# Performance work log

Hardware: AMD Instinct MI355X
Metric: run time of the kernel (lower is better)

The kernel has to match this reference:

```python
import jax, jax.numpy as jnp
import numpy as np

N = 4096            # data_length
T_IN, D_IN = 64, 128
F = 32 * 64         # target_length * output_dim


def setup_inputs() -> dict:
    key = jax.random.key(0)
    k1, k2, k3, k4 = jax.random.split(key, 4)
    xs = jax.random.normal(k1, (N, T_IN, D_IN), dtype=jnp.float32)
    W = jax.random.normal(k2, (T_IN * D_IN, F), dtype=jnp.float32) / np.sqrt(T_IN * D_IN)
    ys = jax.random.randint(k3, (N,), 0, 2, dtype=jnp.int32)  # {0,1} -> mapped to +-1 labels
    alphas = jax.random.normal(k4, (N,), dtype=jnp.float32)
    return {"xs": xs, "W": W, "ys": ys, "alphas": alphas}


def reference(xs, W, ys, alphas):
    gamma = 1.0 / F  # RBF bandwidth
    # encoder (stand-in for seq2seq): [N, T*D] @ [T*D, F] -> [N, F]
    X = xs.reshape(N, -1) @ W
    # pairwise squared distances via gram trick
    sq = jnp.sum(X * X, axis=-1)                       # [N]
    d2 = sq[:, None] + sq[None, :] - 2.0 * (X @ X.T)   # [N, N]
    d2 = jnp.maximum(d2, 0.0)
    K = jnp.exp(-gamma * d2)                           # RBF kernel matrix
    lab = (2 * ys - 1).astype(X.dtype)                 # +-1 labels
    G = (lab[:, None] * lab[None, :]) * K              # gram[i][j] = y_i y_j k(x_i, x_j)
    # 0.5 * alpha^T G alpha - sum(alpha)
    value = 0.5 * jnp.dot(alphas, G @ alphas) - jnp.sum(alphas)
    return value.reshape(1, 1)
```

## Files before the change

kernel.cpp:

```cpp
#include <hip/hip_runtime.h>
#include <hip/hip_bf16.h>

#define N_ROWS 4096
#define K_IN   8192
#define F_DIM  2048
#define GAMMA  (1.0f / 2048.0f)

typedef unsigned short u16;
typedef unsigned int   u32;
typedef unsigned char  u8;
typedef __attribute__((ext_vector_type(4))) int   i32x4;
typedef __attribute__((ext_vector_type(8))) int   i32x8;
typedef __attribute__((ext_vector_type(4))) float f32x4;
typedef __attribute__((ext_vector_type(2))) float f32x2;

__device__ __forceinline__ u32 pk4_fp8(float a, float b, float c, float d) {
  u32 u = 0;
  u = __builtin_amdgcn_cvt_pk_fp8_f32(a, b, u, false);
  u = __builtin_amdgcn_cvt_pk_fp8_f32(c, d, u, true);
  return u;
}
__device__ __forceinline__ u8 f8(float v) {
  return (u8)(__builtin_amdgcn_cvt_pk_fp8_f32(v, v, 0, false) & 0xff);
}

__device__ __forceinline__ void async16(const void* g, void* l) {
  __builtin_amdgcn_global_load_lds(
      (const __attribute__((address_space(1))) void*)g,
      (__attribute__((address_space(3))) void*)l, 16, 0, 0);
}


__global__ void convert_xs(const float4* __restrict__ in, u32* __restrict__ out, int n4) {
  int base = blockIdx.x * (blockDim.x * 4) + threadIdx.x;
#pragma unroll
  for (int k = 0; k < 4; ++k) {
    int i = base + k * 256;
    if (i < n4) {
      float4 v = in[i];
      out[i] = pk4_fp8(v.x, v.y, v.z, v.w);
    }
  }
}

__global__ void transpose_w(const float* __restrict__ W, u8* __restrict__ Wt) {
  __shared__ float tile[128][33];
  int k0 = blockIdx.x * 128;
  int f0 = blockIdx.y * 32;
  int tx = threadIdx.x, ty = threadIdx.y;
#pragma unroll
  for (int kk = 0; kk < 16; ++kk) {
    int k = kk * 8 + ty;
    tile[k][tx] = 64.0f * W[(size_t)(k0 + k) * F_DIM + f0 + tx];
  }
  __syncthreads();
#pragma unroll
  for (int ff = 0; ff < 4; ++ff) {
    int f = ff * 8 + ty;
    int kk = tx * 4;
    u32 p = pk4_fp8(tile[kk][f], tile[kk + 1][f], tile[kk + 2][f], tile[kk + 3][f]);
    *(u32*)(Wt + (size_t)(f0 + f) * K_IN + k0 + kk) = p;
  }
}

__global__ void prep(const float* __restrict__ alphas, const int* __restrict__ ys,
                     float* __restrict__ beta, float* __restrict__ out) {
  __shared__ float red[1024];
  int t = threadIdx.x;
  float s = 0.f;
  for (int i = t; i < N_ROWS; i += 1024) {
    float a = alphas[i];
    beta[i] = a * (float)(2 * ys[i] - 1);
    s += a;
  }
  red[t] = s;
  __syncthreads();
  for (int off = 512; off; off >>= 1) {
    if (t < off) red[t] += red[t + off];
    __syncthreads();
  }
  if (t == 0) out[0] = -red[0];
}

__global__ void row_sq(const u32* __restrict__ X, float* __restrict__ sq) {
  int wave = threadIdx.x >> 6, lane = threadIdx.x & 63;
  int row = blockIdx.x * 4 + wave;
  const uint4* xr = (const uint4*)(X + (size_t)row * (F_DIM / 4));
  float s = 0.f;
#pragma unroll
  for (int it = 0; it < 2; ++it) {
    uint4 v = xr[lane + it * 64];
    u32 w[4] = {v.x, v.y, v.z, v.w};
#pragma unroll
    for (int p = 0; p < 4; ++p) {
      f32x2 lo = __builtin_amdgcn_cvt_pk_f32_fp8(w[p], false);
      f32x2 hi = __builtin_amdgcn_cvt_pk_f32_fp8(w[p], true);
      s += lo[0] * lo[0] + lo[1] * lo[1] + hi[0] * hi[0] + hi[1] * hi[1];
    }
  }
#pragma unroll
  for (int off = 32; off; off >>= 1) s += __shfl_down(s, off);
  if (lane == 0) sq[row] = s;
}


template <int K>
__device__ __forceinline__ void gemm_tile_f8(const u8* __restrict__ A, const u8* __restrict__ Bt,
                                             int m0, int n0, u8* sA, u8* sB, int tid,
                                             int sclA, int sclB, f32x4 acc[4][4]) {
  const int lane = tid & 63;
  const int q = lane >> 4;
  const int r = lane & 15;
  const int wave = tid >> 6;
  const int wm = (wave >> 1) << 6;
  const int wn = (wave & 1) << 6;

  const f32x4 zero = {0.f, 0.f, 0.f, 0.f};
#pragma unroll
  for (int mt = 0; mt < 4; ++mt)
#pragma unroll
    for (int nt = 0; nt < 4; ++nt) acc[mt][nt] = zero;

  int rowS[4], colS[4], offS[4];
#pragma unroll
  for (int j = 0; j < 4; ++j) {
    int o = tid * 16 + j * 4096;
    int row = o >> 7;
    int cb = (o >> 4) & 7;
    rowS[j] = row;
    colS[j] = ((cb ^ (row & 7)) << 4);
    offS[j] = o;
  }

  for (int k0 = 0; k0 < K; k0 += 128) {
#pragma unroll
    for (int j = 0; j < 4; ++j) {
      async16(A + (size_t)(m0 + rowS[j]) * K + k0 + colS[j], sA + offS[j]);
      async16(Bt + (size_t)(n0 + rowS[j]) * K + k0 + colS[j], sB + offS[j]);
    }
    __syncthreads();

    i32x8 af[4], bg[4];
#pragma unroll
    for (int mt = 0; mt < 4; ++mt) {
      int m = wm + (mt << 4) + r;
      i32x4 lo = *(const i32x4*)(sA + m * 128 + ((((q << 1) | 0) ^ (m & 7)) << 4));
      i32x4 hi = *(const i32x4*)(sA + m * 128 + ((((q << 1) | 1) ^ (m & 7)) << 4));
      i32x8 f = {lo[0], lo[1], lo[2], lo[3], hi[0], hi[1], hi[2], hi[3]};
      af[mt] = f;
    }
#pragma unroll
    for (int nt = 0; nt < 4; ++nt) {
      int n = wn + (nt << 4) + r;
      i32x4 lo = *(const i32x4*)(sB + n * 128 + ((((q << 1) | 0) ^ (n & 7)) << 4));
      i32x4 hi = *(const i32x4*)(sB + n * 128 + ((((q << 1) | 1) ^ (n & 7)) << 4));
      i32x8 f = {lo[0], lo[1], lo[2], lo[3], hi[0], hi[1], hi[2], hi[3]};
      bg[nt] = f;
    }
#pragma unroll
    for (int mt = 0; mt < 4; ++mt)
#pragma unroll
      for (int nt = 0; nt < 4; ++nt)
        acc[mt][nt] = __builtin_amdgcn_mfma_scale_f32_16x16x128_f8f6f4(
            af[mt], bg[nt], acc[mt][nt], 0, 0, 0, sclA, 0, sclB);
    __syncthreads();
  }
}

__global__ __launch_bounds__(512, 2) void gemm_xw(const u8* __restrict__ A,
                                                  const u8* __restrict__ Bt,
                                                  u8* __restrict__ X) {
  __shared__ __align__(16) u8 sA[3][256 * 128];
  __shared__ __align__(16) u8 sB[3][128 * 128];
  const int tid = threadIdx.x;
  const int wg = blockIdx.x;
  const int L = (wg & 7) * 32 + (wg >> 3);
  const int m0 = (L & 15) << 8;
  const int n0 = (L >> 4) << 7;

  const int lane = tid & 63;
  const int q = lane >> 4;
  const int r = lane & 15;
  const int wave = tid >> 6;
  const int wm = (wave >> 1) << 6;
  const int wn = (wave & 1) << 6;

  const u8* gA[4]; int oA[4];
  const u8* gB[2]; int oB[2];
#pragma unroll
  for (int j = 0; j < 4; ++j) {
    int o = tid * 16 + j * 8192;
    int row = o >> 7, cb = (o >> 4) & 7;
    oA[j] = o;
    gA[j] = A + (size_t)(m0 + row) * K_IN + ((cb ^ (row & 7)) << 4);
  }
#pragma unroll
  for (int j = 0; j < 2; ++j) {
    int o = tid * 16 + j * 8192;
    int row = o >> 7, cb = (o >> 4) & 7;
    oB[j] = o;
    gB[j] = Bt + (size_t)(n0 + row) * K_IN + ((cb ^ (row & 7)) << 4);
  }

  const int cLo = (((q << 1) | 0) ^ (r & 7)) << 4;
  const int cHi = (((q << 1) | 1) ^ (r & 7)) << 4;
  const int aBase = (wm + r) << 7;
  const int bBase = (wn + r) << 7;

  f32x4 acc[4][4];
  const f32x4 zero = {0.f, 0.f, 0.f, 0.f};
#pragma unroll
  for (int i = 0; i < 4; ++i)
#pragma unroll
    for (int j = 0; j < 4; ++j) acc[i][j] = zero;

#pragma unroll
  for (int j = 0; j < 4; ++j) async16(gA[j], &sA[0][oA[j]]);
#pragma unroll
  for (int j = 0; j < 2; ++j) async16(gB[j], &sB[0][oB[j]]);
#pragma unroll
  for (int j = 0; j < 4; ++j) async16(gA[j] + 128, &sA[1][oA[j]]);
#pragma unroll
  for (int j = 0; j < 2; ++j) async16(gB[j] + 128, &sB[1][oB[j]]);
  asm volatile("s_waitcnt vmcnt(6)" ::: "memory");
  __builtin_amdgcn_s_barrier();

  i32x8 af0, af1, af2, af3, bg0, bg1, bg2, bg3;

#define LDA(FR, MT, BUF) { \
    const u8* b_ = &sA[BUF][aBase + (MT) * 2048]; \
    i32x4 lo_ = *(const i32x4*)(b_ + cLo); \
    i32x4 hi_ = *(const i32x4*)(b_ + cHi); \
    FR = (i32x8){lo_[0], lo_[1], lo_[2], lo_[3], hi_[0], hi_[1], hi_[2], hi_[3]}; }
#define LDB(FR, NT, BUF) { \
    const u8* b_ = &sB[BUF][bBase + (NT) * 2048]; \
    i32x4 lo_ = *(const i32x4*)(b_ + cLo); \
    i32x4 hi_ = *(const i32x4*)(b_ + cHi); \
    FR = (i32x8){lo_[0], lo_[1], lo_[2], lo_[3], hi_[0], hi_[1], hi_[2], hi_[3]}; }
#define MFMA1(MT, NT, AF, BG) \
    acc[MT][NT] = __builtin_amdgcn_mfma_scale_f32_16x16x128_f8f6f4( \
        AF, BG, acc[MT][NT], 0, 0, 0, 127, 0, 121);

  int cur = 0, nb = 2;
  for (int kt = 0; kt < 64; ++kt) {
    const bool st = (kt + 2 < 64);
    const int k2 = (kt + 2) << 7;
    LDA(af0, 0, cur) LDA(af1, 1, cur) LDB(bg0, 0, cur) LDB(bg1, 1, cur)
    if (st) { async16(gA[0] + k2, &sA[nb][oA[0]]); async16(gA[1] + k2, &sA[nb][oA[1]]); }
    __builtin_amdgcn_s_barrier();
    asm volatile("s_waitcnt lgkmcnt(0)" ::: "memory");
    __builtin_amdgcn_sched_barrier(0);
    __builtin_amdgcn_s_setprio(1);
    MFMA1(0, 0, af0, bg0) MFMA1(0, 1, af0, bg1) MFMA1(1, 0, af1, bg0) MFMA1(1, 1, af1, bg1)
    __builtin_amdgcn_s_setprio(0);
    __builtin_amdgcn_s_barrier();
    LDA(af2, 2, cur) LDA(af3, 3, cur)
    if (st) { async16(gA[2] + k2, &sA[nb][oA[2]]); async16(gA[3] + k2, &sA[nb][oA[3]]); }
    __builtin_amdgcn_s_barrier();
    asm volatile("s_waitcnt lgkmcnt(0)" ::: "memory");
    __builtin_amdgcn_sched_barrier(0);
    __builtin_amdgcn_s_setprio(1);
    MFMA1(2, 0, af2, bg0) MFMA1(2, 1, af2, bg1) MFMA1(3, 0, af3, bg0) MFMA1(3, 1, af3, bg1)
    __builtin_amdgcn_s_setprio(0);
    __builtin_amdgcn_s_barrier();
    LDB(bg2, 2, cur) LDB(bg3, 3, cur)
    if (st) { async16(gB[0] + k2, &sB[nb][oB[0]]); async16(gB[1] + k2, &sB[nb][oB[1]]); }
    __builtin_amdgcn_s_barrier();
    asm volatile("s_waitcnt lgkmcnt(0)" ::: "memory");
    __builtin_amdgcn_sched_barrier(0);
    __builtin_amdgcn_s_setprio(1);
    MFMA1(0, 2, af0, bg2) MFMA1(0, 3, af0, bg3) MFMA1(1, 2, af1, bg2) MFMA1(1, 3, af1, bg3)
    __builtin_amdgcn_s_setprio(0);
    __builtin_amdgcn_s_barrier();
    __builtin_amdgcn_s_setprio(1);
    MFMA1(2, 2, af2, bg2) MFMA1(2, 3, af2, bg3) MFMA1(3, 2, af3, bg2) MFMA1(3, 3, af3, bg3)
    __builtin_amdgcn_s_setprio(0);
    if (st) {
      asm volatile("s_waitcnt vmcnt(6)" ::: "memory");
    } else if (kt < 63) {
      asm volatile("s_waitcnt vmcnt(0)" ::: "memory");
    }
    __builtin_amdgcn_s_barrier();
    cur = (cur == 2) ? 0 : cur + 1;
    nb  = (nb == 2) ? 0 : nb + 1;
  }
#undef LDA
#undef LDB
#undef MFMA1

#pragma unroll
  for (int mt = 0; mt < 4; ++mt) {
#pragma unroll
    for (int nt = 0; nt < 4; ++nt) {
      int row = m0 + wm + (mt << 4) + (q << 2);
      int col = n0 + wn + (nt << 4) + r;
#pragma unroll
      for (int e = 0; e < 4; ++e)
        X[(size_t)(row + e) * F_DIM + col] = f8(acc[mt][nt][e]);
    }
  }
}

__global__ __launch_bounds__(256, 3) void gemm_kern(const u8* __restrict__ X,
                                                    const float* __restrict__ sq,
                                                    const float* __restrict__ beta,
                                                    float* __restrict__ out) {
  __shared__ __align__(16) u8 sA[128 * 128];
  __shared__ __align__(16) u8 sB[128 * 128];
  const int tid = threadIdx.x;
  int bid = blockIdx.x;
  int ib = 0;
  while (bid >= 32 - ib) { bid -= 32 - ib; ++ib; }
  const int jb = ib + bid;
  const int m0 = ib << 7;
  const int n0 = jb << 7;

  f32x4 acc[4][4];
  gemm_tile_f8<F_DIM>(X, X, m0, n0, sA, sB, tid, 127, 127, acc);

  const int lane = tid & 63;
  const int q = lane >> 4;
  const int r = lane & 15;
  const int wave = tid >> 6;
  const int wm = (wave >> 1) << 6;
  const int wn = (wave & 1) << 6;

  float sqj[4], bj[4];
#pragma unroll
  for (int nt = 0; nt < 4; ++nt) {
    int j = n0 + wn + (nt << 4) + r;
    sqj[nt] = sq[j];
    bj[nt] = beta[j];
  }
  float local = 0.f;
#pragma unroll
  for (int mt = 0; mt < 4; ++mt) {
#pragma unroll
    for (int e = 0; e < 4; ++e) {
      int i = m0 + wm + (mt << 4) + (q << 2) + e;
      float sqi = sq[i];
      float bi = beta[i];
#pragma unroll
      for (int nt = 0; nt < 4; ++nt) {
        float d2 = fmaxf(sqi + sqj[nt] - 2.f * acc[mt][nt][e], 0.f);
        local += bi * bj[nt] * __expf(-GAMMA * d2);
      }
    }
  }
  local *= (ib == jb) ? 0.5f : 1.0f;
#pragma unroll
  for (int off = 32; off; off >>= 1) local += __shfl_down(local, off);
  if (lane == 0) atomicAdd(out, local);
}


extern "C" void kernel_launch(void* const* d_in, const int* in_sizes, int n_in,
                              void* d_out, int out_size, void* d_ws, size_t ws_size,
                              hipStream_t stream) {
  const float* xs = (const float*)d_in[0];
  const float* W = (const float*)d_in[1];
  const int* ys = (const int*)d_in[2];
  const float* alphas = (const float*)d_in[3];
  float* out = (float*)d_out;

  char* ws = (char*)d_ws;
  u8* xs_f8 = (u8*)ws;
  u8* Wt_f8 = (u8*)(ws + 33554432);
  u8* X_f8  = (u8*)(ws + 50331648);
  float* sq   = (float*)(ws + 58720256);
  float* beta = (float*)(ws + 58736640);

  convert_xs<<<8192, 256, 0, stream>>>((const float4*)xs, (u32*)xs_f8,
                                       (N_ROWS * K_IN) / 4);
  dim3 tb(32, 8);
  dim3 tg(K_IN / 128, F_DIM / 32);
  transpose_w<<<tg, tb, 0, stream>>>(W, Wt_f8);
  prep<<<1, 1024, 0, stream>>>(alphas, ys, beta, out);

  gemm_xw<<<256, 512, 0, stream>>>(xs_f8, Wt_f8, X_f8);
  row_sq<<<N_ROWS / 4, 256, 0, stream>>>((const u32*)X_f8, sq);
  gemm_kern<<<528, 256, 0, stream>>>(X_f8, sq, beta, out);
}
```

Before: 371.1 us.

## Restructure XW GEMM to 128x256 tiles with 4 waves and simplified pipeline

The XW GEMM changes from 512-thread blocks with 256x128 tiles (8 waves as 4x2) to 256-thread blocks with 128x256 tiles, where each of the 4 waves owns a 128x64 slab. The inner loop drops the interleaved barrier/setprio phases in favour of one prefetch-all stage and a software-pipelined loop over 8 A fragments. Each wave now holds twice as many accumulators, which raises register pressure and limits the launch to one block per SM. Fewer barriers per k-step may cut sync overhead, but the loss of occupancy could expose LDS and global latency.

```diff
diff --git a/kernel.cpp b/kernel.cpp
--- a/kernel.cpp
+++ b/kernel.cpp
@@ -167,36 +167,35 @@
   }
 }
 
-__global__ __launch_bounds__(512, 2) void gemm_xw(const u8* __restrict__ A,
+__global__ __launch_bounds__(256, 1) void gemm_xw(const u8* __restrict__ A,
                                                   const u8* __restrict__ Bt,
                                                   u8* __restrict__ X) {
-  __shared__ __align__(16) u8 sA[3][256 * 128];
-  __shared__ __align__(16) u8 sB[3][128 * 128];
+  __shared__ __align__(16) u8 sA[3][128 * 128];
+  __shared__ __align__(16) u8 sB[3][256 * 128];
   const int tid = threadIdx.x;
   const int wg = blockIdx.x;
   const int L = (wg & 7) * 32 + (wg >> 3);
-  const int m0 = (L & 15) << 8;
-  const int n0 = (L >> 4) << 7;
+  const int m0 = (L & 31) << 7;
+  const int n0 = (L >> 5) << 8;
 
   const int lane = tid & 63;
   const int q = lane >> 4;
   const int r = lane & 15;
   const int wave = tid >> 6;
-  const int wm = (wave >> 1) << 6;
-  const int wn = (wave & 1) << 6;
+  const int wn = wave << 6;
 
   const u8* gA[4]; int oA[4];
-  const u8* gB[2]; int oB[2];
+  const u8* gB[8]; int oB[8];
 #pragma unroll
   for (int j = 0; j < 4; ++j) {
-    int o = tid * 16 + j * 8192;
+    int o = tid * 16 + j * 4096;
     int row = o >> 7, cb = (o >> 4) & 7;
     oA[j] = o;
     gA[j] = A + (size_t)(m0 + row) * K_IN + ((cb ^ (row & 7)) << 4);
   }
 #pragma unroll
-  for (int j = 0; j < 2; ++j) {
-    int o = tid * 16 + j * 8192;
+  for (int j = 0; j < 8; ++j) {
+    int o = tid * 16 + j * 4096;
     int row = o >> 7, cb = (o >> 4) & 7;
     oB[j] = o;
     gB[j] = Bt + (size_t)(n0 + row) * K_IN + ((cb ^ (row & 7)) << 4);
@@ -204,35 +203,34 @@
 
   const int cLo = (((q << 1) | 0) ^ (r & 7)) << 4;
   const int cHi = (((q << 1) | 1) ^ (r & 7)) << 4;
-  const int aBase = (wm + r) << 7;
+  const int aBase = r << 7;
   const int bBase = (wn + r) << 7;
 
-  f32x4 acc[4][4];
+  f32x4 acc[8][4];
   const f32x4 zero = {0.f, 0.f, 0.f, 0.f};
 #pragma unroll
-  for (int i = 0; i < 4; ++i)
+  for (int i = 0; i < 8; ++i)
 #pragma unroll
     for (int j = 0; j < 4; ++j) acc[i][j] = zero;
 
-#pragma unroll
-  for (int j = 0; j < 4; ++j) async16(gA[j], &sA[0][oA[j]]);
-#pragma unroll
-  for (int j = 0; j < 2; ++j) async16(gB[j], &sB[0][oB[j]]);
-#pragma unroll
-  for (int j = 0; j < 4; ++j) async16(gA[j] + 128, &sA[1][oA[j]]);
-#pragma unroll
-  for (int j = 0; j < 2; ++j) async16(gB[j] + 128, &sB[1][oB[j]]);
-  asm volatile("s_waitcnt vmcnt(6)" ::: "memory");
+#define STAGE(BUF, KOFF) { \
+    _Pragma("unroll") for (int j_ = 0; j_ < 4; ++j_) \
+      async16(gA[j_] + (KOFF), &sA[BUF][oA[j_]]); \
+    _Pragma("unroll") for (int j_ = 0; j_ < 8; ++j_) \
+      async16(gB[j_] + (KOFF), &sB[BUF][oB[j_]]); }
+
+  STAGE(0, 0)
+  STAGE(1, 128)
+  asm volatile("s_waitcnt vmcnt(12)" ::: "memory");
   __builtin_amdgcn_s_barrier();
-
-  i32x8 af0, af1, af2, af3, bg0, bg1, bg2, bg3;
-
-#define LDA(FR, MT, BUF) { \
+  __builtin_amdgcn_sched_barrier(0);
+
+#define LDAf(FR, MT, BUF) { \
     const u8* b_ = &sA[BUF][aBase + (MT) * 2048]; \
     i32x4 lo_ = *(const i32x4*)(b_ + cLo); \
     i32x4 hi_ = *(const i32x4*)(b_ + cHi); \
     FR = (i32x8){lo_[0], lo_[1], lo_[2], lo_[3], hi_[0], hi_[1], hi_[2], hi_[3]}; }
-#define LDB(FR, NT, BUF) { \
+#define LDBf(FR, NT, BUF) { \
     const u8* b_ = &sB[BUF][bBase + (NT) * 2048]; \
     i32x4 lo_ = *(const i32x4*)(b_ + cLo); \
     i32x4 hi_ = *(const i32x4*)(b_ + cHi); \
@@ -244,55 +242,43 @@
   int cur = 0, nb = 2;
   for (int kt = 0; kt < 64; ++kt) {
     const bool st = (kt + 2 < 64);
-    const int k2 = (kt + 2) << 7;
-    LDA(af0, 0, cur) LDA(af1, 1, cur) LDB(bg0, 0, cur) LDB(bg1, 1, cur)
-    if (st) { async16(gA[0] + k2, &sA[nb][oA[0]]); async16(gA[1] + k2, &sA[nb][oA[1]]); }
-    __builtin_amdgcn_s_barrier();
-    asm volatile("s_waitcnt lgkmcnt(0)" ::: "memory");
-    __builtin_amdgcn_sched_barrier(0);
-    __builtin_amdgcn_s_setprio(1);
-    MFMA1(0, 0, af0, bg0) MFMA1(0, 1, af0, bg1) MFMA1(1, 0, af1, bg0) MFMA1(1, 1, af1, bg1)
-    __builtin_amdgcn_s_setprio(0);
-    __builtin_amdgcn_s_barrier();
-    LDA(af2, 2, cur) LDA(af3, 3, cur)
-    if (st) { async16(gA[2] + k2, &sA[nb][oA[2]]); async16(gA[3] + k2, &sA[nb][oA[3]]); }
-    __builtin_amdgcn_s_barrier();
-    asm volatile("s_waitcnt lgkmcnt(0)" ::: "memory");
-    __builtin_amdgcn_sched_barrier(0);
-    __builtin_amdgcn_s_setprio(1);
-    MFMA1(2, 0, af2, bg0) MFMA1(2, 1, af2, bg1) MFMA1(3, 0, af3, bg0) MFMA1(3, 1, af3, bg1)
-    __builtin_amdgcn_s_setprio(0);
-    __builtin_amdgcn_s_barrier();
-    LDB(bg2, 2, cur) LDB(bg3, 3, cur)
-    if (st) { async16(gB[0] + k2, &sB[nb][oB[0]]); async16(gB[1] + k2, &sB[nb][oB[1]]); }
-    __builtin_amdgcn_s_barrier();
-    asm volatile("s_waitcnt lgkmcnt(0)" ::: "memory");
-    __builtin_amdgcn_sched_barrier(0);
-    __builtin_amdgcn_s_setprio(1);
-    MFMA1(0, 2, af0, bg2) MFMA1(0, 3, af0, bg3) MFMA1(1, 2, af1, bg2) MFMA1(1, 3, af1, bg3)
-    __builtin_amdgcn_s_setprio(0);
-    __builtin_amdgcn_s_barrier();
-    __builtin_amdgcn_s_setprio(1);
-    MFMA1(2, 2, af2, bg2) MFMA1(2, 3, af2, bg3) MFMA1(3, 2, af3, bg2) MFMA1(3, 3, af3, bg3)
-    __builtin_amdgcn_s_setprio(0);
+    if (st) { const int k2 = (kt + 2) << 7; STAGE(nb, k2) }
+
+    i32x8 bg[4];
+#pragma unroll
+    for (int nt = 0; nt < 4; ++nt) LDBf(bg[nt], nt, cur)
+    i32x8 af[8];
+    LDAf(af[0], 0, cur)
+    LDAf(af[1], 1, cur)
+#pragma unroll
+    for (int mt = 0; mt < 8; ++mt) {
+      if (mt + 2 < 8) LDAf(af[mt + 2], mt + 2, cur)
+      MFMA1(mt, 0, af[mt], bg[0])
+      MFMA1(mt, 1, af[mt], bg[1])
+      MFMA1(mt, 2, af[mt], bg[2])
+      MFMA1(mt, 3, af[mt], bg[3])
+    }
+
     if (st) {
-      asm volatile("s_waitcnt vmcnt(6)" ::: "memory");
+      asm volatile("s_waitcnt vmcnt(12)" ::: "memory");
     } else if (kt < 63) {
       asm volatile("s_waitcnt vmcnt(0)" ::: "memory");
     }
     __builtin_amdgcn_s_barrier();
+    __builtin_amdgcn_sched_barrier(0);
     cur = (cur == 2) ? 0 : cur + 1;
     nb  = (nb == 2) ? 0 : nb + 1;
   }
-#undef LDA
-#undef LDB
+#undef STAGE
+#undef LDAf
+#undef LDBf
 #undef MFMA1
 
 #pragma unroll
-  for (int mt = 0; mt < 4; ++mt) {
+  for (int mt = 0; mt < 8; ++mt) {
 #pragma unroll
     for (int nt = 0; nt < 4; ++nt) {
-      int row = m0 + wm + (mt << 4) + (q << 2);
+      int row = m0 + (mt << 4) + (q << 2);
       int col = n0 + wn + (nt << 4) + r;
 #pragma unroll
       for (int e = 0; e < 4; ++e)
@@ -377,7 +363,7 @@
   transpose_w<<<tg, tb, 0, stream>>>(W, Wt_f8);
   prep<<<1, 1024, 0, stream>>>(alphas, ys, beta, out);
 
-  gemm_xw<<<256, 512, 0, stream>>>(xs_f8, Wt_f8, X_f8);
+  gemm_xw<<<256, 256, 0, stream>>>(xs_f8, Wt_f8, X_f8);
   row_sq<<<N_ROWS / 4, 256, 0, stream>>>((const u32*)X_f8, sq);
   gemm_kern<<<528, 256, 0, stream>>>(X_f8, sq, beta, out);
 }
```

Result: slower. 406.9 us (+9.7%).
